# Performance work log

Hardware: AMD Instinct MI355X
Metric: run time of the kernel (lower is better)

The kernel has to match this reference:

```python
import jax, jax.numpy as jnp
import numpy as np


def setup_inputs() -> dict:
    key = jax.random.key(0)
    k_v, k_w, k_b, k_c = jax.random.split(key, 4)
    B, V, H = 32768, 1024, 128
    # Binary visible input, as RBM_BB (Bernoulli-Bernoulli) expects
    v_0 = (jax.random.uniform(k_v, (B, V, 1)) < 0.5).astype(jnp.float32)
    W = 0.01 * jax.random.normal(k_w, (H, V), dtype=jnp.float32)
    b = 0.01 * jax.random.normal(k_b, (V, 1), dtype=jnp.float32)
    c = 0.01 * jax.random.normal(k_c, (H, 1), dtype=jnp.float32)
    return {"v_0": v_0, "W": W, "b": b, "c": c, "num_sampling_iter": 4}


def reference(v_0, W, b, c, num_sampling_iter):
    """Block Gibbs sampling for a Bernoulli-Bernoulli RBM.

    v: [B, V, 1], h: [B, H, 1]; W: [H, V], b: [V, 1], c: [H, 1].
    Returns (v_given_h, h_given_v, h_given_v_0), all detached samples.
    """
    dtype = v_0.dtype
    key = jax.random.key(42)

    def p_h_given_v(v):  # [B,V,1] -> [B,H,1]
        return jax.nn.sigmoid(jnp.matmul(W, v) + c)

    def p_v_given_h(h):  # [B,H,1] -> [B,V,1]
        return jax.nn.sigmoid(jnp.matmul(W.T, h) + b)

    def bernoulli(k, p):
        # sample is detached (torch .detach()) -> stop_gradient
        return jax.lax.stop_gradient(jax.random.bernoulli(k, p).astype(dtype))

    keys = jax.random.split(key, num_sampling_iter + 1)
    h_given_v_0 = bernoulli(keys[0], p_h_given_v(v_0))

    def gibbs_step(h, k):
        k_v, k_h = jax.random.split(k)
        v = bernoulli(k_v, p_v_given_h(h))
        h_new = bernoulli(k_h, p_h_given_v(v))
        return h_new, v

    h_given_v, vs = jax.lax.scan(gibbs_step, h_given_v_0, keys[1:])
    v_given_h = vs[-1]
    return (v_given_h, h_given_v, h_given_v_0)
```

## Files before the change

kernel.cpp:

```cpp
#include <hip/hip_runtime.h>
#include <cstdint>


#define TF_ROT(x, r) (((x) << (r)) | ((x) >> (32 - (r))))

__host__ __device__ __forceinline__ void threefry2x32(
    uint32_t k0, uint32_t k1, uint32_t x0, uint32_t x1,
    uint32_t &o0, uint32_t &o1) {
  const uint32_t ks2 = k0 ^ k1 ^ 0x1BD11BDAu;
  x0 += k0; x1 += k1;
#define TF_R(r) { x0 += x1; x1 = TF_ROT(x1, r); x1 ^= x0; }
  TF_R(13) TF_R(15) TF_R(26) TF_R(6)
  x0 += k1; x1 += ks2 + 1u;
  TF_R(17) TF_R(29) TF_R(16) TF_R(24)
  x0 += ks2; x1 += k0 + 2u;
  TF_R(13) TF_R(15) TF_R(26) TF_R(6)
  x0 += k0; x1 += k1 + 3u;
  TF_R(17) TF_R(29) TF_R(16) TF_R(24)
  x0 += k1; x1 += ks2 + 4u;
  TF_R(13) TF_R(15) TF_R(26) TF_R(6)
  x0 += ks2; x1 += k0 + 5u;
#undef TF_R
  o0 = x0; o1 = x1;
}

__device__ __forceinline__ float cephes_expf(float xin) {
  float xc = fminf(xin, 88.3762626647950f);
  xc = fmaxf(xc, -88.3762626647949f);
  float fx = floorf(xc * 1.44269504088896341f + 0.5f);
  float tmp = 0.693359375f * fx;
  float z2  = -2.12194440e-4f * fx;
  float x = xc - tmp;
  x = x - z2;
  float z = x * x;
  float y = 1.9875691500E-4f * x + 1.3981999507E-3f;
  y = y * x + 8.3334519073E-3f;
  y = y * x + 4.1665795894E-2f;
  y = y * x + 1.6666665459E-1f;
  y = y * x + 5.0000001201E-1f;
  y = y * z + x;
  y = 1.0f + y;
  int n = (int)fx;
  float p2n = __uint_as_float((uint32_t)(n + 127) << 23);
  return fmaxf(y * p2n, xin);
}

__device__ __forceinline__ void sample_store(
    float tot, const float* bias, float* out,
    long b, int ng, int N_total, uint32_t k0, uint32_t k1) {
  float pre = tot + bias[ng];
  float p   = 1.0f / (1.0f + cephes_expf(-pre));
  uint32_t flat = (uint32_t)(b * N_total + ng);
  uint32_t w0, w1;
  threefry2x32(k0, k1, 0u, flat, w0, w1);
  uint32_t bits = w0 ^ w1;
  float u = __uint_as_float((bits >> 9) | 0x3f800000u) - 1.0f;
  out[(long)b * N_total + ng] = (u < p) ? 1.0f : 0.0f;
}

#define LSTRIDE 36

template <bool SAMPLE, bool SINGLE_PANEL>
__global__ __launch_bounds__(256, 4) void gemm_tile(
    const float* __restrict__ A,
    const float* __restrict__ Bt,
    const float* __restrict__ bias,
    float* __restrict__ out,
    int ldA, int N_total, int K, int tiles_per_panel, int Mtot,
    uint32_t k0, uint32_t k1)
{
  __shared__ float As[64 * LSTRIDE];
  __shared__ float Bs[128 * LSTRIDE];
  const int t  = threadIdx.x;
  const int tx = t & 15;
  const int ty = t >> 4;
  const int bm = blockIdx.x;
  const int j0 = blockIdx.y << 7;

  int kb, ke;
  float* outp = out;
  if (SAMPLE) { kb = 0; ke = K; }
  else {
    const int z = blockIdx.z;
    kb = z * 320;
    ke = min(K, kb + 320);
    outp = out + (size_t)z * Mtot * 128;
  }

  float cur[4][8];
  float tot[4][8];
#pragma unroll
  for (int i = 0; i < 4; ++i)
#pragma unroll
    for (int j = 0; j < 8; ++j) { cur[i][j] = 0.0f; if (!SINGLE_PANEL) tot[i][j] = 0.0f; }

  const long arow = (long)bm * 64 * ldA;
  const int t0 = kb >> 5, t1 = ke >> 5;

  const float* aP = As + ty * LSTRIDE;
  const float* bP = Bs + tx * LSTRIDE;

  for (int tki = t0; tki < t1; ++tki) {
    const int kc = tki << 5;
#pragma unroll
    for (int r = 0; r < 2; ++r) {
      int q = t + 256 * r;
      int m = q >> 3;
      int c = q & 7;
      float4 val = *(const float4*)(A + arow + (long)m * ldA + kc + 4 * c);
      *(float4*)(As + m * LSTRIDE + 4 * c) = val;
    }
#pragma unroll
    for (int r = 0; r < 4; ++r) {
      int q = t + 256 * r;
      int n = q >> 3;
      int c = q & 7;
      float4 val = *(const float4*)(Bt + (long)(j0 + n) * ldA + kc + 4 * c);
      *(float4*)(Bs + n * LSTRIDE + 4 * c) = val;
    }
    __syncthreads();

#pragma unroll
    for (int c = 0; c < 8; ++c) {
      float4 av[4], bv[8];
#pragma unroll
      for (int i = 0; i < 4; ++i)
        av[i] = *(const float4*)(aP + i * 16 * LSTRIDE + 4 * c);
#pragma unroll
      for (int j = 0; j < 8; ++j)
        bv[j] = *(const float4*)(bP + j * 16 * LSTRIDE + 4 * c);
#pragma unroll
      for (int i = 0; i < 4; ++i)
#pragma unroll
        for (int j = 0; j < 8; ++j) {
          cur[i][j] = __fmaf_rn(av[i].x, bv[j].x, cur[i][j]);
          cur[i][j] = __fmaf_rn(av[i].y, bv[j].y, cur[i][j]);
          cur[i][j] = __fmaf_rn(av[i].z, bv[j].z, cur[i][j]);
          cur[i][j] = __fmaf_rn(av[i].w, bv[j].w, cur[i][j]);
        }
    }
    __syncthreads();

    if (!SINGLE_PANEL) {
      if (((tki - t0 + 1) % tiles_per_panel == 0) || (tki == t1 - 1)) {
#pragma unroll
        for (int i = 0; i < 4; ++i)
#pragma unroll
          for (int j = 0; j < 8; ++j) { tot[i][j] += cur[i][j]; cur[i][j] = 0.0f; }
      }
    }
  }

#pragma unroll
  for (int i = 0; i < 4; ++i) {
    const int m = ty + 16 * i;
    const long b = (long)bm * 64 + m;
#pragma unroll
    for (int j = 0; j < 8; ++j) {
      const int n  = tx + 16 * j;
      const int ng = j0 + n;
      const float v = SINGLE_PANEL ? cur[i][j] : tot[i][j];
      if (SAMPLE) {
        sample_store(v, bias, outp, b, ng, N_total, k0, k1);
      } else {
        outp[b * 128 + ng] = v;
      }
    }
  }
}

__global__ __launch_bounds__(256) void combine_sample(
    const float* __restrict__ partials,
    const float* __restrict__ bias,
    float* __restrict__ out,
    int Mtot, uint32_t k0, uint32_t k1)
{
  const long idx = (long)blockIdx.x * 256 + threadIdx.x;
  const long S = (long)Mtot * 128;
  float p0 = partials[idx];
  float p1 = partials[S + idx];
  float p2 = partials[2 * S + idx];
  float p3 = partials[3 * S + idx];
  float tot = ((p0 + p1) + p2) + p3;
  float pre = tot + bias[(int)(idx & 127)];
  float p   = 1.0f / (1.0f + cephes_expf(-pre));
  uint32_t w0, w1;
  threefry2x32(k0, k1, 0u, (uint32_t)idx, w0, w1);
  uint32_t bits = w0 ^ w1;
  float u = __uint_as_float((bits >> 9) | 0x3f800000u) - 1.0f;
  out[idx] = (u < p) ? 1.0f : 0.0f;
}

__global__ void transpose_W(const float* __restrict__ W, float* __restrict__ Wt) {
  __shared__ float tile[32][33];
  int bx = blockIdx.x, by = blockIdx.y;
  int x = threadIdx.x, y = threadIdx.y;
  tile[y][x] = W[(by * 32 + y) * 1024 + bx * 32 + x];
  __syncthreads();
  Wt[(bx * 32 + y) * 128 + by * 32 + x] = tile[x][y];
}

extern "C" void kernel_launch(void* const* d_in, const int* in_sizes, int n_in,
                              void* d_out, int out_size, void* d_ws, size_t ws_size,
                              hipStream_t stream) {
  const float* v0 = (const float*)d_in[0];
  const float* W  = (const float*)d_in[1];
  const float* bb = (const float*)d_in[2];
  const float* cb = (const float*)d_in[3];
  const int B = in_sizes[0] / 1024;

  float* out    = (float*)d_out;
  float* out_v  = out;
  float* out_h1 = out + (size_t)B * 1024;
  float* out_h2 = out_h1 + (size_t)B * 128;

  float* Wt       = (float*)d_ws;
  float* h_ws     = Wt + 1024 * 128;
  float* partials = h_ws + (size_t)B * 128;
  const size_t need = (size_t)(1024 * 128 + (size_t)B * 128 * 5) * 4;
  const bool use_split = ws_size >= need;

  uint32_t kt[5][2], kv[5][2], kh[5][2];
  for (uint32_t i = 0; i < 5; ++i) threefry2x32(0u, 42u, 0u, i, kt[i][0], kt[i][1]);
  for (int t = 1; t <= 4; ++t) {
    threefry2x32(kt[t][0], kt[t][1], 0u, 0u, kv[t][0], kv[t][1]);
    threefry2x32(kt[t][0], kt[t][1], 0u, 1u, kh[t][0], kh[t][1]);
  }

  transpose_W<<<dim3(32, 4), dim3(32, 32), 0, stream>>>(W, Wt);

  const int MB = B / 64;

  auto h_step = [&](const float* vin, float* hdst, uint32_t hk0, uint32_t hk1) {
    if (use_split) {
      gemm_tile<false, true><<<dim3(MB, 1, 4), 256, 0, stream>>>(
          vin, W, nullptr, partials, 1024, 128, 1024, 1000, B, 0u, 0u);
      combine_sample<<<dim3(B * 128 / 256), 256, 0, stream>>>(
          partials, cb, hdst, B, hk0, hk1);
    } else {
      gemm_tile<true, false><<<dim3(MB, 1, 1), 256, 0, stream>>>(
          vin, W, cb, hdst, 1024, 128, 1024, 10, B, hk0, hk1);
    }
  };

  h_step(v0, out_h2, kt[0][0], kt[0][1]);

  const float* h = out_h2;
  for (int t = 1; t <= 4; ++t) {
    gemm_tile<true, true><<<dim3(MB, 8, 1), 256, 0, stream>>>(
        h, Wt, bb, out_v, 128, 1024, 128, 10, B, kv[t][0], kv[t][1]);
    float* hdst = (t == 4) ? out_h1 : h_ws;
    h_step(out_v, hdst, kh[t][0], kh[t][1]);
    h = hdst;
  }
}
```

Measured before the change: 1.638 ms.

## Double-buffer GEMM shared tiles with register prefetch and drop trailing barrier

```diff
diff --git a/kernel.cpp b/kernel.cpp
--- a/kernel.cpp
+++ b/kernel.cpp
@@ -58,7 +58,8 @@
   out[(long)b * N_total + ng] = (u < p) ? 1.0f : 0.0f;
 }
 
-#define LSTRIDE 36
+#define AST 34
+#define BST 34
 
 template <bool SAMPLE, bool SINGLE_PANEL>
 __global__ __launch_bounds__(256, 4) void gemm_tile(
@@ -69,8 +70,8 @@
     int ldA, int N_total, int K, int tiles_per_panel, int Mtot,
     uint32_t k0, uint32_t k1)
 {
-  __shared__ float As[64 * LSTRIDE];
-  __shared__ float Bs[128 * LSTRIDE];
+  __shared__ float As[2][64 * AST];
+  __shared__ float Bs[2][128 * BST];
   const int t  = threadIdx.x;
   const int tx = t & 15;
   const int ty = t >> 4;
@@ -97,38 +98,59 @@
   const long arow = (long)bm * 64 * ldA;
   const int t0 = kb >> 5, t1 = ke >> 5;
 
-  const float* aP = As + ty * LSTRIDE;
-  const float* bP = Bs + tx * LSTRIDE;
-
-  for (int tki = t0; tki < t1; ++tki) {
-    const int kc = tki << 5;
-#pragma unroll
-    for (int r = 0; r < 2; ++r) {
-      int q = t + 256 * r;
-      int m = q >> 3;
-      int c = q & 7;
-      float4 val = *(const float4*)(A + arow + (long)m * ldA + kc + 4 * c);
-      *(float4*)(As + m * LSTRIDE + 4 * c) = val;
-    }
+  const int am0 = t >> 3,           ac0 = t & 7;
+  const int am1 = (t + 256) >> 3,   ac1 = ac0;
+  const int bn0 = t >> 3,           bc0 = t & 7;
+
+  float4 aReg[2], bReg[4];
+
+  {
+    const int kc = t0 << 5;
+    aReg[0] = *(const float4*)(A + arow + (long)am0 * ldA + kc + 4 * ac0);
+    aReg[1] = *(const float4*)(A + arow + (long)am1 * ldA + kc + 4 * ac1);
 #pragma unroll
     for (int r = 0; r < 4; ++r) {
       int q = t + 256 * r;
-      int n = q >> 3;
-      int c = q & 7;
-      float4 val = *(const float4*)(Bt + (long)(j0 + n) * ldA + kc + 4 * c);
-      *(float4*)(Bs + n * LSTRIDE + 4 * c) = val;
+      int n = q >> 3, c = q & 7;
+      bReg[r] = *(const float4*)(Bt + (long)(j0 + n) * ldA + kc + 4 * c);
+    }
+  }
+
+  int pp = 0;
+  for (int tki = t0; tki < t1; ++tki) {
+    *(float4*)(As[pp] + am0 * AST + 4 * ac0) = aReg[0];
+    *(float4*)(As[pp] + am1 * AST + 4 * ac1) = aReg[1];
+#pragma unroll
+    for (int r = 0; r < 4; ++r) {
+      int q = t + 256 * r;
+      int n = q >> 3, c = q & 7;
+      *(float4*)(Bs[pp] + n * BST + 4 * c) = bReg[r];
     }
     __syncthreads();
 
+    if (tki + 1 < t1) {
+      const int kc = (tki + 1) << 5;
+      aReg[0] = *(const float4*)(A + arow + (long)am0 * ldA + kc + 4 * ac0);
+      aReg[1] = *(const float4*)(A + arow + (long)am1 * ldA + kc + 4 * ac1);
+#pragma unroll
+      for (int r = 0; r < 4; ++r) {
+        int q = t + 256 * r;
+        int n = q >> 3, c = q & 7;
+        bReg[r] = *(const float4*)(Bt + (long)(j0 + n) * ldA + kc + 4 * c);
+      }
+    }
+
+    const float* aP = As[pp] + ty * AST;
+    const float* bP = Bs[pp] + tx * BST;
 #pragma unroll
     for (int c = 0; c < 8; ++c) {
       float4 av[4], bv[8];
 #pragma unroll
       for (int i = 0; i < 4; ++i)
-        av[i] = *(const float4*)(aP + i * 16 * LSTRIDE + 4 * c);
+        av[i] = *(const float4*)(aP + i * 16 * AST + 4 * c);
 #pragma unroll
       for (int j = 0; j < 8; ++j)
-        bv[j] = *(const float4*)(bP + j * 16 * LSTRIDE + 4 * c);
+        bv[j] = *(const float4*)(bP + j * 16 * BST + 4 * c);
 #pragma unroll
       for (int i = 0; i < 4; ++i)
 #pragma unroll
@@ -139,7 +161,6 @@
           cur[i][j] = __fmaf_rn(av[i].w, bv[j].w, cur[i][j]);
         }
     }
-    __syncthreads();
 
     if (!SINGLE_PANEL) {
       if (((tki - t0 + 1) % tiles_per_panel == 0) || (tki == t1 - 1)) {
@@ -149,6 +170,7 @@
           for (int j = 0; j < 8; ++j) { tot[i][j] += cur[i][j]; cur[i][j] = 0.0f; }
       }
     }
+    pp ^= 1;
   }
 
 #pragma unroll
```

Measured after the change: 5.823 ms. 3.56x slower.
